# Kernel optimization log

Hardware: AMD Instinct MI355X
Metric: run time of the kernel (lower is better)

The kernel has to match this reference:

```python
import jax, jax.numpy as jnp
import numpy as np

DIM = 2048
LAT = 512          # dim / compression_factor
NH = 16
NKV = 4
HD = LAT // NH     # 32
KVD = NKV * HD     # 128
K = 3              # conv kernel
GAIN = 0.25
EPS = 1e-6
THETA = 10000.0


def _rms(x, g):
    x32 = x.astype(jnp.float32)
    r = jax.lax.rsqrt(jnp.mean(x32 * x32, axis=-1, keepdims=True) + EPS)
    return (x32 * r).astype(x.dtype) * g.astype(x.dtype)


def _causal_conv(x, w, groups):
    # x: [B,S,C], w: [C, C//groups, K]; left-pad K-1 == pad both + trim right
    xc = jnp.transpose(x, (0, 2, 1))
    y = jax.lax.conv_general_dilated(
        xc, w, window_strides=(1,), padding=[(K - 1, 0)],
        feature_group_count=groups, dimension_numbers=('NCH', 'OIH', 'NCH'))
    return jnp.transpose(y, (0, 2, 1))


def _rope_tables(S):
    freqs = 1.0 / THETA ** (jnp.arange(0, HD, 2, dtype=jnp.float32) / HD)
    t = jnp.arange(S, dtype=jnp.float32)
    f = jnp.outer(t, freqs)               # [S, HD/2]
    return jnp.cos(f), jnp.sin(f)


def _rope(x, cos, sin):
    # x: [B,H,S,HD]; interleaved even/odd rotation
    x1, x2 = x[..., ::2], x[..., 1::2]
    r1 = x1 * cos - x2 * sin
    r2 = x1 * sin + x2 * cos
    return jnp.stack([r1, r2], axis=-1).reshape(x.shape)


def setup_inputs() -> dict:
    key = jax.random.key(0)
    ks = jax.random.split(key, 8)
    s = 0.02
    return {
        'x': jax.random.normal(ks[0], (4, 2048, DIM), jnp.float32),
        'w_q': jax.random.normal(ks[1], (LAT, DIM), jnp.float32) * s,
        'w_k': jax.random.normal(ks[2], (KVD, DIM), jnp.float32) * s,
        'w_v': jax.random.normal(ks[3], (KVD, DIM), jnp.float32) * s,
        'g_latent': jnp.ones((LAT,), jnp.float32),
        'g_kv': jnp.ones((KVD,), jnp.float32),
        'conv_q_w': jax.random.normal(ks[4], (LAT, LAT // NH, K), jnp.float32) * s,
        'conv_k_w': jax.random.normal(ks[5], (KVD, KVD // NKV, K), jnp.float32) * s,
        'g_conv': jnp.ones((LAT,), jnp.float32),
        'g_kconv': jnp.ones((KVD,), jnp.float32),
        'g_postq': jnp.ones((LAT,), jnp.float32),
        'g_postk': jnp.ones((KVD,), jnp.float32),
        'key_temp': jnp.ones((1,), jnp.float32),
        'g_preout': jnp.ones((LAT,), jnp.float32),
        'w_o': jax.random.normal(ks[6], (DIM, LAT), jnp.float32) * s,
    }


def reference(x, w_q, w_k, w_v, g_latent, g_kv, conv_q_w, conv_k_w,
              g_conv, g_kconv, g_postq, g_postk, key_temp, g_preout, w_o):
    B, S, D = x.shape
    n_groups = NH // NKV

    q = _rms(x @ w_q.T, g_latent)          # [B,S,LAT]
    k = _rms(x @ w_k.T, g_kv)              # [B,S,KVD]
    v = _rms(x @ w_v.T, g_kv)
    q_pre, k_pre = q, k

    q = _rms(_causal_conv(q, conv_q_w, NH), g_conv)
    k = _rms(_causal_conv(k, conv_k_w, NKV), g_kconv)

    # qk-mean modulation (n_groups > 1 branch)
    q_mean = q_pre.reshape(B, S, NH, HD).mean(axis=2)    # [B,S,HD]
    k_mean = k_pre.reshape(B, S, NKV, HD).mean(axis=2)   # [B,S,HD]
    q = q + GAIN * jnp.broadcast_to(k_mean[:, :, None, :], (B, S, NH, HD)).reshape(B, S, LAT)
    k = k + GAIN * jnp.broadcast_to(q_mean[:, :, None, :], (B, S, NKV, HD)).reshape(B, S, KVD)

    q = _rms(q, g_postq)
    k = _rms(k, g_postk)

    q = q.reshape(B, S, NH, HD).transpose(0, 2, 1, 3)    # [B,NH,S,HD]
    k = k.reshape(B, S, NKV, HD).transpose(0, 2, 1, 3)   # [B,NKV,S,HD]
    v = v.reshape(B, S, NKV, HD).transpose(0, 2, 1, 3)

    # QK L2 norm with learnable key temperature
    sqrt_hd = jnp.sqrt(jnp.float32(HD))
    qn = jnp.maximum(jnp.linalg.norm(q, axis=-1, keepdims=True), 1e-12)
    kn = jnp.maximum(jnp.linalg.norm(k, axis=-1, keepdims=True), 1e-12)
    q = q / qn * sqrt_hd
    k = k / kn * sqrt_hd * key_temp[0]

    cos, sin = _rope_tables(S)
    q = _rope(q, cos, sin)
    k = _rope(k, cos, sin)

    # GQA expand kv heads
    k = jnp.broadcast_to(k[:, :, None], (B, NKV, n_groups, S, HD)).reshape(B, NH, S, HD)
    v = jnp.broadcast_to(v[:, :, None], (B, NKV, n_groups, S, HD)).reshape(B, NH, S, HD)

    scale = HD ** -0.5
    scores = jnp.einsum('bhqd,bhkd->bhqk', q, k) * scale
    causal = jnp.tril(jnp.ones((S, S), bool))
    scores = jnp.where(causal, scores, jnp.finfo(scores.dtype).min)
    attn = jax.nn.softmax(scores, axis=-1)
    out = jnp.einsum('bhqk,bhkd->bhqd', attn, v)

    out = out.transpose(0, 2, 1, 3).reshape(B, S, LAT)
    out = _rms(out, g_preout)
    return out @ w_o.T
```

## Files before the change

### kernel.cpp

```cpp
#include <hip/hip_runtime.h>
#include <hip/hip_bf16.h>
#include <math.h>

constexpr int S_LEN = 2048;
constexpr int B_SZ  = 4;
constexpr int NROWS = B_SZ * S_LEN;
constexpr float GAIN_  = 0.25f;
constexpr float EPS_   = 1e-6f;
constexpr float THETA_ = 10000.0f;
constexpr float LOG2E_ = 1.44269504f;

typedef __attribute__((ext_vector_type(8))) short short8;
typedef __attribute__((ext_vector_type(4))) short sshort4;
typedef __attribute__((ext_vector_type(4))) float float4v;

__device__ __forceinline__ short f2bs(float f) {
    __hip_bfloat16 h = __float2bfloat16(f);
    short r;
    __builtin_memcpy(&r, &h, 2);
    return r;
}

__device__ __forceinline__ float bs2f(short s) {
    unsigned u = ((unsigned)(unsigned short)s) << 16;
    float f;
    __builtin_memcpy(&f, &u, 4);
    return f;
}

__device__ __forceinline__ void async_copy16(const short* g, short* l) {
    __builtin_amdgcn_global_load_lds(
        (const __attribute__((address_space(1))) void*)g,
        (__attribute__((address_space(3))) void*)l, 16, 0, 0);
}

__device__ __forceinline__ int xcd_remap(int nwg) {
    int orig = blockIdx.x + gridDim.x * (blockIdx.y + gridDim.y * blockIdx.z);
    return (orig & 7) * (nwg >> 3) + (orig >> 3);
}

__device__ __forceinline__ float block_reduce_sum_256(float v, float* scratch) {
    __syncthreads();
    for (int off = 32; off > 0; off >>= 1)
        v += __shfl_down(v, off, 64);
    int lane = threadIdx.x & 63;
    int wid  = threadIdx.x >> 6;
    if (lane == 0) scratch[wid] = v;
    __syncthreads();
    return scratch[0] + scratch[1] + scratch[2] + scratch[3];
}

__device__ __forceinline__ void block_reduce_sum2_256(float& a, float& b, float* scratch) {
    __syncthreads();
    for (int off = 32; off > 0; off >>= 1) {
        a += __shfl_down(a, off, 64);
        b += __shfl_down(b, off, 64);
    }
    int lane = threadIdx.x & 63;
    int wid  = threadIdx.x >> 6;
    if (lane == 0) { scratch[wid] = a; scratch[4 + wid] = b; }
    __syncthreads();
    a = scratch[0] + scratch[1] + scratch[2] + scratch[3];
    b = scratch[4] + scratch[5] + scratch[6] + scratch[7];
}

__device__ __forceinline__ void block_reduce_sum3_256(float& a, float& b, float& c, float* scratch) {
    __syncthreads();
    for (int off = 32; off > 0; off >>= 1) {
        a += __shfl_down(a, off, 64);
        b += __shfl_down(b, off, 64);
        c += __shfl_down(c, off, 64);
    }
    int lane = threadIdx.x & 63;
    int wid  = threadIdx.x >> 6;
    if (lane == 0) { scratch[wid] = a; scratch[4 + wid] = b; scratch[8 + wid] = c; }
    __syncthreads();
    a = scratch[0] + scratch[1] + scratch[2] + scratch[3];
    b = scratch[4] + scratch[5] + scratch[6] + scratch[7];
    c = scratch[8] + scratch[9] + scratch[10] + scratch[11];
}

__global__ __launch_bounds__(256) void cvt_bf16(
    const float* __restrict__ src, short* __restrict__ dst, int n) {
    int i = (blockIdx.x * 256 + threadIdx.x) * 4;
    if (i >= n) return;
    float4 v = *(const float4*)(src + i);
    sshort4 o;
    o.x = f2bs(v.x); o.y = f2bs(v.y); o.z = f2bs(v.z); o.w = f2bs(v.w);
    *(sshort4*)(dst + i) = o;
}

__global__ __launch_bounds__(256) void cvt_weights(
    const float* __restrict__ wq, const float* __restrict__ wk,
    const float* __restrict__ wv, const float* __restrict__ wo,
    short* __restrict__ wqkvb, short* __restrict__ wob) {
    int i = (blockIdx.x * 256 + threadIdx.x) * 4;
    const float* src;
    short* dst;
    int j;
    if (i < 1048576)      { src = wq; dst = wqkvb + i; j = i; }
    else if (i < 1310720) { src = wk; dst = wqkvb + i; j = i - 1048576; }
    else if (i < 1572864) { src = wv; dst = wqkvb + i; j = i - 1310720; }
    else                  { src = wo; dst = wob + (i - 1572864); j = i - 1572864; }
    float4 v = *(const float4*)(src + j);
    sshort4 o;
    o.x = f2bs(v.x); o.y = f2bs(v.y); o.z = f2bs(v.z); o.w = f2bs(v.w);
    *(sshort4*)dst = o;
}

__global__ __launch_bounds__(256) void rope_tab(float* __restrict__ tab) {
    int i = blockIdx.x * 256 + threadIdx.x;
    int s = i >> 4, fi = i & 15;
    float freq = powf(THETA_, -(float)fi / 16.f);
    float sn, cs;
    sincosf((float)s * freq, &sn, &cs);
    tab[i * 2]     = cs;
    tab[i * 2 + 1] = sn;
}

__global__ __launch_bounds__(256) void gemm_bf16_mfma(
    const short* __restrict__ A, const short* __restrict__ B,
    float* __restrict__ C, int N, int K) {
    __shared__ short As[128 * 32];
    __shared__ short Bs[128 * 32];
    int tid = threadIdx.x;
    int wave = tid >> 6, lane = tid & 63;
    int wg = xcd_remap(gridDim.x * gridDim.y);
    int bx = wg % gridDim.x, by = wg / gridDim.x;
    int m0 = by * 128, n0 = bx * 128;
    int wm = (wave >> 1) * 64, wn = (wave & 1) * 64;
    int mrow = lane & 15, quad = lane >> 4;
    float4v acc[4][4] = {};
    for (int k0 = 0; k0 < K; k0 += 32) {
        __syncthreads();
#pragma unroll
        for (int p = 0; p < 2; ++p) {
            int f = p * 256 + tid;
            int row = f >> 2, ch = (f & 3) * 8;
            const short* ga = A + (size_t)(m0 + row) * K + k0 + ch;
            const short* gb = B + (size_t)(n0 + row) * K + k0 + ch;
            async_copy16(ga, As + p * 2048 + wave * 512);
            async_copy16(gb, Bs + p * 2048 + wave * 512);
        }
        __syncthreads();
        short8 af[4], bf[4];
#pragma unroll
        for (int i = 0; i < 4; ++i)
            af[i] = *(const short8*)&As[(wm + i * 16 + mrow) * 32 + quad * 8];
#pragma unroll
        for (int j = 0; j < 4; ++j)
            bf[j] = *(const short8*)&Bs[(wn + j * 16 + mrow) * 32 + quad * 8];
#pragma unroll
        for (int i = 0; i < 4; ++i)
#pragma unroll
            for (int j = 0; j < 4; ++j)
                acc[i][j] = __builtin_amdgcn_mfma_f32_16x16x32_bf16(af[i], bf[j], acc[i][j], 0, 0, 0);
    }
#pragma unroll
    for (int i = 0; i < 4; ++i)
#pragma unroll
        for (int r = 0; r < 4; ++r) {
            int m = m0 + wm + i * 16 + quad * 4 + r;
            float* crow = C + (size_t)m * N + n0 + wn;
#pragma unroll
            for (int j = 0; j < 4; ++j)
                crow[j * 16 + mrow] = acc[i][j][r];
        }
}

__global__ __launch_bounds__(256) void gemm_bf16_mfma_sk2(
    const short* __restrict__ A, const short* __restrict__ B,
    float* __restrict__ C0, float* __restrict__ C1, int N, int K) {
    __shared__ short As[128 * 32];
    __shared__ short Bs[128 * 32];
    int tid = threadIdx.x;
    int wave = tid >> 6, lane = tid & 63;
    int wg = xcd_remap(gridDim.x * gridDim.y * gridDim.z);
    int bx = wg % gridDim.x;
    int t  = wg / gridDim.x;
    int by = t % gridDim.y;
    int bz = t / gridDim.y;
    int m0 = by * 128, n0 = bx * 128;
    int wm = (wave >> 1) * 64, wn = (wave & 1) * 64;
    int mrow = lane & 15, quad = lane >> 4;
    int kh = K >> 1;
    int kbeg = bz * kh, kend = kbeg + kh;
    float* __restrict__ C = bz ? C1 : C0;
    float4v acc[4][4] = {};
    for (int k0 = kbeg; k0 < kend; k0 += 32) {
        __syncthreads();
#pragma unroll
        for (int p = 0; p < 2; ++p) {
            int f = p * 256 + tid;
            int row = f >> 2, ch = (f & 3) * 8;
            const short* ga = A + (size_t)(m0 + row) * K + k0 + ch;
            const short* gb = B + (size_t)(n0 + row) * K + k0 + ch;
            async_copy16(ga, As + p * 2048 + wave * 512);
            async_copy16(gb, Bs + p * 2048 + wave * 512);
        }
        __syncthreads();
        short8 af[4], bf[4];
#pragma unroll
        for (int i = 0; i < 4; ++i)
            af[i] = *(const short8*)&As[(wm + i * 16 + mrow) * 32 + quad * 8];
#pragma unroll
        for (int j = 0; j < 4; ++j)
            bf[j] = *(const short8*)&Bs[(wn + j * 16 + mrow) * 32 + quad * 8];
#pragma unroll
        for (int i = 0; i < 4; ++i)
#pragma unroll
            for (int j = 0; j < 4; ++j)
                acc[i][j] = __builtin_amdgcn_mfma_f32_16x16x32_bf16(af[i], bf[j], acc[i][j], 0, 0, 0);
    }
#pragma unroll
    for (int i = 0; i < 4; ++i)
#pragma unroll
        for (int r = 0; r < 4; ++r) {
            int m = m0 + wm + i * 16 + quad * 4 + r;
            float* crow = C + (size_t)m * N + n0 + wn;
#pragma unroll
            for (int j = 0; j < 4; ++j)
                crow[j * 16 + mrow] = acc[i][j][r];
        }
}

__global__ __launch_bounds__(256) void rms_qkv_means(
    float* __restrict__ qkv, const float* __restrict__ qkv2,
    const float* __restrict__ g_latent, const float* __restrict__ g_kv,
    float* __restrict__ qmean, float* __restrict__ kmean,
    short* __restrict__ vtb) {
    int row = blockIdx.x;
    int b = row >> 11, s = row & (S_LEN - 1);
    float* p = qkv + (size_t)row * 768;
    const float* p2 = qkv2 + (size_t)row * 768;
    __shared__ float sh[640];
    __shared__ float scratch[12];
    int tid = threadIdx.x;
    float v0 = p[tid] + p2[tid];
    float v1 = p[tid + 256] + p2[tid + 256];
    float v2 = p[tid + 512] + p2[tid + 512];
    float sq = v0 * v0 + v1 * v1;
    float sk = (tid < 128) ? v2 * v2 : 0.f;
    float sv = (tid >= 128) ? v2 * v2 : 0.f;
    block_reduce_sum3_256(sq, sk, sv, scratch);
    float rq = rsqrtf(sq / 512.f + EPS_);
    float q0 = v0 * rq * g_latent[tid];
    float q1 = v1 * rq * g_latent[tid + 256];
    p[tid] = q0; p[tid + 256] = q1;
    sh[tid] = q0; sh[tid + 256] = q1;
    if (tid < 128) {
        float rk = rsqrtf(sk / 128.f + EPS_);
        float kv = v2 * rk * g_kv[tid];
        p[512 + tid] = kv; sh[512 + tid] = kv;
    } else {
        float rv = rsqrtf(sv / 128.f + EPS_);
        float vv = v2 * rv * g_kv[tid - 128];
        int d_full = tid - 128;
        vtb[((size_t)(b * 4 + (d_full >> 5)) * 32 + (d_full & 31)) * S_LEN + s] = f2bs(vv);
    }
    __syncthreads();
    if (tid < 32) {
        float sm = 0.f;
#pragma unroll
        for (int h = 0; h < 16; ++h) sm += sh[h * 32 + tid];
        qmean[(size_t)row * 32 + tid] = sm * (1.f / 16.f);
    } else if (tid < 64) {
        int d = tid - 32;
        float sm = 0.f;
#pragma unroll
        for (int h = 0; h < 4; ++h) sm += sh[512 + h * 32 + d];
        kmean[(size_t)row * 32 + d] = sm * 0.25f;
    }
}

__global__ __launch_bounds__(256) void causal_conv32(
    const float* __restrict__ in, int ldin, int inoff,
    const float* __restrict__ w, float* __restrict__ out, int C) {
    int b = blockIdx.z, g = blockIdx.y, s0 = blockIdx.x * 32;
    __shared__ float wsh[32][3][32];
    __shared__ float ish[34][33];
    int tid = threadIdx.x;
    for (int i = tid; i < 32 * 96; i += 256) {
        int oc = i / 96, r = i % 96;
        wsh[r / 3][r % 3][oc] = w[(size_t)(g * 32 + oc) * 96 + r];
    }
    for (int i = tid; i < 34 * 32; i += 256) {
        int pp = i >> 5, ic = i & 31;
        int s = s0 - 2 + pp;
        ish[pp][ic] = (s >= 0) ? in[((size_t)b * S_LEN + s) * ldin + inoff + g * 32 + ic] : 0.f;
    }
    __syncthreads();
    int sl = tid >> 3, oc0 = (tid & 7) * 4;
    float acc[4] = {0.f, 0.f, 0.f, 0.f};
    for (int ic = 0; ic < 32; ++ic) {
        float x0 = ish[sl][ic], x1 = ish[sl + 1][ic], x2 = ish[sl + 2][ic];
#pragma unroll
        for (int j = 0; j < 4; ++j)
            acc[j] += x0 * wsh[ic][0][oc0 + j] + x1 * wsh[ic][1][oc0 + j] + x2 * wsh[ic][2][oc0 + j];
    }
    float* orow = out + ((size_t)b * S_LEN + s0 + sl) * C + g * 32 + oc0;
    orow[0] = acc[0]; orow[1] = acc[1]; orow[2] = acc[2]; orow[3] = acc[3];
}

__global__ __launch_bounds__(256) void mix_rows(
    const float* __restrict__ convq, const float* __restrict__ convk,
    const float* __restrict__ qmean, const float* __restrict__ kmean,
    const float* __restrict__ g_conv, const float* __restrict__ g_kconv,
    const float* __restrict__ g_postq, const float* __restrict__ g_postk,
    const float* __restrict__ key_temp, const float* __restrict__ rtab,
    short* __restrict__ qb, short* __restrict__ kb) {
    int row = blockIdx.x;
    int s = row & (S_LEN - 1);
    int tid = threadIdx.x;
    __shared__ float sh[640];
    __shared__ float scratch[8];
    __shared__ float hscale[20];
    float q0 = convq[(size_t)row * 512 + tid];
    float q1 = convq[(size_t)row * 512 + tid + 256];
    float k0 = (tid < 128) ? convk[(size_t)row * 128 + tid] : 0.f;
    float ssq = q0 * q0 + q1 * q1;
    float ssk = k0 * k0;
    block_reduce_sum2_256(ssq, ssk, scratch);
    float r1  = rsqrtf(ssq / 512.f + EPS_);
    float rk1 = rsqrtf(ssk / 128.f + EPS_);
    float km = kmean[(size_t)row * 32 + (tid & 31)];
    float a0 = q0 * r1 * g_conv[tid] + GAIN_ * km;
    float a1 = q1 * r1 * g_conv[tid + 256] + GAIN_ * km;
    float ak = 0.f;
    if (tid < 128) ak = k0 * rk1 * g_kconv[tid] + GAIN_ * qmean[(size_t)row * 32 + (tid & 31)];
    float ssq2 = a0 * a0 + a1 * a1;
    float ssk2 = ak * ak;
    block_reduce_sum2_256(ssq2, ssk2, scratch);
    float r2  = rsqrtf(ssq2 / 512.f + EPS_);
    float rk2 = rsqrtf(ssk2 / 128.f + EPS_);
    sh[tid] = a0 * r2 * g_postq[tid];
    sh[tid + 256] = a1 * r2 * g_postq[tid + 256];
    if (tid < 128) sh[512 + tid] = ak * rk2 * g_postk[tid];
    __syncthreads();
    if (tid < 16) {
        float ssh = 0.f;
        for (int d = 0; d < 32; ++d) { float x = sh[tid * 32 + d]; ssh += x * x; }
        hscale[tid] = LOG2E_ / fmaxf(sqrtf(ssh), 1e-12f);
    } else if (tid < 20) {
        int h = tid - 16;
        float ssh = 0.f;
        for (int d = 0; d < 32; ++d) { float x = sh[512 + h * 32 + d]; ssh += x * x; }
        hscale[tid] = sqrtf(32.f) / fmaxf(sqrtf(ssh), 1e-12f) * key_temp[0];
    }
    __syncthreads();
    {
        int i0 = tid * 2;
        int h = i0 >> 5;
        int fi = (i0 & 31) >> 1;
        float sc = hscale[h];
        float x1 = sh[i0] * sc, x2 = sh[i0 + 1] * sc;
        float2 cssn = *(const float2*)&rtab[((size_t)s * 16 + fi) * 2];
        float cs = cssn.x, sn = cssn.y;
        unsigned lo = (unsigned short)f2bs(x1 * cs - x2 * sn);
        unsigned hi = (unsigned short)f2bs(x1 * sn + x2 * cs);
        *(unsigned*)(qb + (size_t)row * 512 + i0) = lo | (hi << 16);
    }
    if (tid < 64) {
        int i0 = tid * 2;
        int h = i0 >> 5;
        int fi = (i0 & 31) >> 1;
        float sc = hscale[16 + h];
        float x1 = sh[512 + i0] * sc, x2 = sh[512 + i0 + 1] * sc;
        float2 cssn = *(const float2*)&rtab[((size_t)s * 16 + fi) * 2];
        float cs = cssn.x, sn = cssn.y;
        unsigned lo = (unsigned short)f2bs(x1 * cs - x2 * sn);
        unsigned hi = (unsigned short)f2bs(x1 * sn + x2 * cs);
        *(unsigned*)(kb + (size_t)row * 128 + i0) = lo | (hi << 16);
    }
}

__global__ __launch_bounds__(256) void attn_mfma(
    const short* __restrict__ qb, const short* __restrict__ kb,
    const short* __restrict__ vtb, short* __restrict__ obf,
    const float* __restrict__ key_temp) {
    int pair = blockIdx.x, h = blockIdx.y, b = blockIdx.z;
    int kvh = h >> 2;
    __shared__ short KF[2][2048];
    __shared__ short VF[2][2048];
    __shared__ __align__(16) short PF[4 * 16 * 72];
    int tid = threadIdx.x, wave = tid >> 6, lane = tid & 63;
    int cc = lane & 15, quad = lane >> 4;
    short* PFw = PF + wave * 16 * 72;
    int ldsoff = wave * 512;
    float shift2 = -5.6568543f * key_temp[0] * LOG2E_;
    float4v zinit = {shift2, shift2, shift2, shift2};
    short8 ones;
#pragma unroll
    for (int j = 0; j < 8; ++j) ones[j] = (short)0x3F80;

    const short* ksrc0 = kb +
        ((size_t)(b * S_LEN + wave * 16 + (tid & 15)) * 128
         + kvh * 32 + ((tid >> 4) & 3) * 8);
    const short* vsrc0 = vtb +
        ((size_t)((b * 4 + kvh) * 32 + (wave & 1) * 16 + (tid & 15)) * S_LEN
         + (tid >> 7) * 32 + ((tid >> 4) & 3) * 8);

    for (int half = 0; half < 2; ++half) {
        int qt = half ? (31 - pair) : pair;
        int s0 = qt * 64;
        short8 qfrag = *(const short8*)(qb +
            ((size_t)(b * S_LEN + s0 + wave * 16 + cc) * 512 + h * 32 + quad * 8));
        float4v accO[2];
        accO[0] = (float4v){0.f, 0.f, 0.f, 0.f};
        accO[1] = (float4v){0.f, 0.f, 0.f, 0.f};
        float4v accL = (float4v){0.f, 0.f, 0.f, 0.f};
        int qpos = s0 + wave * 16 + cc;
        const short* ksrc = ksrc0;
        const short* vsrc = vsrc0;
        int nkt = qt + 1;

        __syncthreads();
        int cur = 0;
        async_copy16(ksrc, KF[0] + ldsoff);
        async_copy16(vsrc, VF[0] + ldsoff);
        ksrc += 64 * 128;
        vsrc += 64;
        for (int kt = 0; kt < nkt; ++kt) {
            __syncthreads();
            if (kt + 1 < nkt) {
                async_copy16(ksrc, KF[cur ^ 1] + ldsoff);
                async_copy16(vsrc, VF[cur ^ 1] + ldsoff);
                ksrc += 64 * 128;
                vsrc += 64;
            }
            const short* KFc = KF[cur];
            const short* VFc = VF[cur];

            float4v st[4];
#pragma unroll
            for (int chunk = 0; chunk < 4; ++chunk) {
                short8 kfrag = *(const short8*)&KFc[chunk * 512 + lane * 8];
                st[chunk] = __builtin_amdgcn_mfma_f32_16x16x32_bf16(kfrag, qfrag, zinit, 0, 0, 0);
            }

            bool diag = (kt == qt);
#pragma unroll
            for (int chunk = 0; chunk < 4; ++chunk) {
                float pv[4];
#pragma unroll
                for (int r = 0; r < 4; ++r) {
                    float e = exp2f(st[chunk][r]);
                    if (diag) {
                        int kpos = kt * 64 + chunk * 16 + quad * 4 + r;
                        e = (kpos <= qpos) ? e : 0.f;
                    }
                    pv[r] = e;
                }
                unsigned u0, u1;
                asm("v_cvt_pk_bf16_f32 %0, %1, %2" : "=v"(u0) : "v"(pv[0]), "v"(pv[1]));
                asm("v_cvt_pk_bf16_f32 %0, %1, %2" : "=v"(u1) : "v"(pv[2]), "v"(pv[3]));
                *(uint2*)&PFw[cc * 72 + chunk * 16 + quad * 4] = make_uint2(u0, u1);
            }

#pragma unroll
            for (int kc = 0; kc < 2; ++kc) {
                short8 pfrag = *(const short8*)&PFw[cc * 72 + kc * 32 + quad * 8];
                accL = __builtin_amdgcn_mfma_f32_16x16x32_bf16(pfrag, ones, accL, 0, 0, 0);
#pragma unroll
                for (int dc = 0; dc < 2; ++dc) {
                    short8 vfrag = *(const short8*)&VFc[(kc * 2 + dc) * 512 + lane * 8];
                    accO[dc] = __builtin_amdgcn_mfma_f32_16x16x32_bf16(pfrag, vfrag, accO[dc], 0, 0, 0);
                }
            }
            cur ^= 1;
        }

#pragma unroll
        for (int r = 0; r < 4; ++r) {
            float linv = 1.f / accL[r];
            short* dst = obf +
                ((size_t)(b * S_LEN + s0 + wave * 16 + quad * 4 + r) * 512 + h * 32 + cc);
            dst[0]  = f2bs(accO[0][r] * linv);
            dst[16] = f2bs(accO[1][r] * linv);
        }
    }
}

__global__ __launch_bounds__(256) void rms_preout_bf16(
    const short* __restrict__ obf, const float* __restrict__ g,
    short* __restrict__ outb) {
    int row = blockIdx.x;
    __shared__ float scratch[4];
    int tid = threadIdx.x;
    unsigned pk = *(const unsigned*)(obf + (size_t)row * 512 + tid * 2);
    float v0 = bs2f((short)(pk & 0xFFFF));
    float v1 = bs2f((short)(pk >> 16));
    float ssq = block_reduce_sum_256(v0 * v0 + v1 * v1, scratch);
    float r = rsqrtf(ssq / 512.f + EPS_);
    unsigned lo = (unsigned short)f2bs(v0 * r * g[tid * 2]);
    unsigned hi = (unsigned short)f2bs(v1 * r * g[tid * 2 + 1]);
    *(unsigned*)(outb + (size_t)row * 512 + tid * 2) = lo | (hi << 16);
}

extern "C" void kernel_launch(void* const* d_in, const int* in_sizes, int n_in,
                              void* d_out, int out_size, void* d_ws, size_t ws_size,
                              hipStream_t stream) {
    (void)in_sizes; (void)n_in; (void)out_size; (void)ws_size;
    const float* x        = (const float*)d_in[0];
    const float* w_q      = (const float*)d_in[1];
    const float* w_k      = (const float*)d_in[2];
    const float* w_v      = (const float*)d_in[3];
    const float* g_latent = (const float*)d_in[4];
    const float* g_kv     = (const float*)d_in[5];
    const float* conv_q_w = (const float*)d_in[6];
    const float* conv_k_w = (const float*)d_in[7];
    const float* g_conv   = (const float*)d_in[8];
    const float* g_kconv  = (const float*)d_in[9];
    const float* g_postq  = (const float*)d_in[10];
    const float* g_postk  = (const float*)d_in[11];
    const float* key_temp = (const float*)d_in[12];
    const float* g_preout = (const float*)d_in[13];
    const float* w_o      = (const float*)d_in[14];
    float* out = (float*)d_out;

    char* ws = (char*)d_ws;
    const size_t R = NROWS;
    float* qkv   = (float*)ws;                        ws += R * 768 * 4;
    float* qmean = (float*)ws;                        ws += R * 32 * 4;
    float* kmean = (float*)ws;                        ws += R * 32 * 4;
    float* convq = (float*)ws;                        ws += R * 512 * 4;
    float* convk = (float*)ws;                        ws += R * 128 * 4;
    short* qbb   = (short*)ws;                        ws += R * 512 * 2;
    short* kbb   = (short*)ws;                        ws += R * 128 * 2;
    short* vtb   = (short*)ws;                        ws += R * 128 * 2;
    short* xb    = (short*)ws;                        ws += R * 2048 * 2;
    short* wqkvb = (short*)ws;                        ws += 768 * 2048 * 2;
    short* w_ob  = (short*)ws;                        ws += 2048 * 512 * 2;
    float* rtab  = (float*)ws;                        ws += 2048 * 16 * 2 * 4;
    float* qkv2  = convq;
    short* obf   = xb;
    short* attnb = xb + R * 512;

    dim3 blk(256);
    rope_tab<<<128, blk, 0, stream>>>(rtab);
    cvt_bf16<<<(NROWS * 2048) / 1024, blk, 0, stream>>>(x, xb, NROWS * 2048);
    cvt_weights<<<2560, blk, 0, stream>>>(w_q, w_k, w_v, w_o, wqkvb, w_ob);

    gemm_bf16_mfma_sk2<<<dim3(6, 64, 2), blk, 0, stream>>>(xb, wqkvb, qkv, qkv2, 768, 2048);
    rms_qkv_means<<<NROWS, blk, 0, stream>>>(qkv, qkv2, g_latent, g_kv, qmean, kmean, vtb);
    causal_conv32<<<dim3(64, 16, 4), blk, 0, stream>>>(qkv, 768, 0, conv_q_w, convq, 512);
    causal_conv32<<<dim3(64, 4, 4), blk, 0, stream>>>(qkv, 768, 512, conv_k_w, convk, 128);
    mix_rows<<<NROWS, blk, 0, stream>>>(convq, convk, qmean, kmean, g_conv, g_kconv,
                                        g_postq, g_postk, key_temp, rtab, qbb, kbb);
    attn_mfma<<<dim3(16, 16, 4), blk, 0, stream>>>(qbb, kbb, vtb, obf, key_temp);
    rms_preout_bf16<<<NROWS, blk, 0, stream>>>(obf, g_preout, attnb);
    gemm_bf16_mfma<<<dim3(16, 64), blk, 0, stream>>>(attnb, w_ob, out, 2048, 512);
}
```

Before: 365.7 us.

## Merge conversion and conv launches; triple-buffer K/V loads in attention

```diff
diff --git a/kernel.cpp b/kernel.cpp
--- a/kernel.cpp
+++ b/kernel.cpp
@@ -80,42 +80,42 @@
     c = scratch[8] + scratch[9] + scratch[10] + scratch[11];
 }
 
-__global__ __launch_bounds__(256) void cvt_bf16(
-    const float* __restrict__ src, short* __restrict__ dst, int n) {
-    int i = (blockIdx.x * 256 + threadIdx.x) * 4;
-    if (i >= n) return;
-    float4 v = *(const float4*)(src + i);
-    sshort4 o;
-    o.x = f2bs(v.x); o.y = f2bs(v.y); o.z = f2bs(v.z); o.w = f2bs(v.w);
-    *(sshort4*)(dst + i) = o;
-}
-
-__global__ __launch_bounds__(256) void cvt_weights(
+__global__ __launch_bounds__(256) void cvt_all(
+    const float* __restrict__ x, short* __restrict__ xb,
     const float* __restrict__ wq, const float* __restrict__ wk,
     const float* __restrict__ wv, const float* __restrict__ wo,
-    short* __restrict__ wqkvb, short* __restrict__ wob) {
-    int i = (blockIdx.x * 256 + threadIdx.x) * 4;
-    const float* src;
-    short* dst;
-    int j;
-    if (i < 1048576)      { src = wq; dst = wqkvb + i; j = i; }
-    else if (i < 1310720) { src = wk; dst = wqkvb + i; j = i - 1048576; }
-    else if (i < 1572864) { src = wv; dst = wqkvb + i; j = i - 1310720; }
-    else                  { src = wo; dst = wob + (i - 1572864); j = i - 1572864; }
-    float4 v = *(const float4*)(src + j);
-    sshort4 o;
-    o.x = f2bs(v.x); o.y = f2bs(v.y); o.z = f2bs(v.z); o.w = f2bs(v.w);
-    *(sshort4*)dst = o;
-}
-
-__global__ __launch_bounds__(256) void rope_tab(float* __restrict__ tab) {
-    int i = blockIdx.x * 256 + threadIdx.x;
-    int s = i >> 4, fi = i & 15;
-    float freq = powf(THETA_, -(float)fi / 16.f);
-    float sn, cs;
-    sincosf((float)s * freq, &sn, &cs);
-    tab[i * 2]     = cs;
-    tab[i * 2 + 1] = sn;
+    short* __restrict__ wqkvb, short* __restrict__ wob,
+    float* __restrict__ rtab) {
+    int blk = blockIdx.x;
+    int tid = threadIdx.x;
+    if (blk < 16384) {
+        int i = (blk * 256 + tid) * 4;
+        float4 v = *(const float4*)(x + i);
+        sshort4 o;
+        o.x = f2bs(v.x); o.y = f2bs(v.y); o.z = f2bs(v.z); o.w = f2bs(v.w);
+        *(sshort4*)(xb + i) = o;
+    } else if (blk < 16384 + 2560) {
+        int i = ((blk - 16384) * 256 + tid) * 4;
+        const float* src;
+        short* dst;
+        int j;
+        if (i < 1048576)      { src = wq; dst = wqkvb + i; j = i; }
+        else if (i < 1310720) { src = wk; dst = wqkvb + i; j = i - 1048576; }
+        else if (i < 1572864) { src = wv; dst = wqkvb + i; j = i - 1310720; }
+        else                  { src = wo; dst = wob + (i - 1572864); j = i - 1572864; }
+        float4 v = *(const float4*)(src + j);
+        sshort4 o;
+        o.x = f2bs(v.x); o.y = f2bs(v.y); o.z = f2bs(v.z); o.w = f2bs(v.w);
+        *(sshort4*)dst = o;
+    } else {
+        int i = (blk - 16384 - 2560) * 256 + tid;
+        int s = i >> 4, fi = i & 15;
+        float freq = powf(THETA_, -(float)fi / 16.f);
+        float sn, cs;
+        sincosf((float)s * freq, &sn, &cs);
+        rtab[i * 2]     = cs;
+        rtab[i * 2 + 1] = sn;
+    }
 }
 
 __global__ __launch_bounds__(256) void gemm_bf16_mfma(
@@ -273,10 +273,10 @@
     }
 }
 
-__global__ __launch_bounds__(256) void causal_conv32(
+__device__ __forceinline__ void conv32_body(
     const float* __restrict__ in, int ldin, int inoff,
-    const float* __restrict__ w, float* __restrict__ out, int C) {
-    int b = blockIdx.z, g = blockIdx.y, s0 = blockIdx.x * 32;
+    const float* __restrict__ w, float* __restrict__ out, int C, int g) {
+    int b = blockIdx.z, s0 = blockIdx.x * 32;
     __shared__ float wsh[32][3][32];
     __shared__ float ish[34][33];
     int tid = threadIdx.x;
@@ -300,6 +300,15 @@
     }
     float* orow = out + ((size_t)b * S_LEN + s0 + sl) * C + g * 32 + oc0;
     orow[0] = acc[0]; orow[1] = acc[1]; orow[2] = acc[2]; orow[3] = acc[3];
+}
+
+__global__ __launch_bounds__(256) void causal_conv_all(
+    const float* __restrict__ qkv, const float* __restrict__ conv_q_w,
+    const float* __restrict__ conv_k_w, float* __restrict__ convq,
+    float* __restrict__ convk) {
+    int y = blockIdx.y;
+    if (y < 16) conv32_body(qkv, 768, 0,   conv_q_w, convq, 512, y);
+    else        conv32_body(qkv, 768, 512, conv_k_w, convk, 128, y - 16);
 }
 
 __global__ __launch_bounds__(256) void mix_rows(
@@ -380,8 +389,8 @@
     const float* __restrict__ key_temp) {
     int pair = blockIdx.x, h = blockIdx.y, b = blockIdx.z;
     int kvh = h >> 2;
-    __shared__ short KF[2][2048];
-    __shared__ short VF[2][2048];
+    __shared__ short KF[3][2048];
+    __shared__ short VF[3][2048];
     __shared__ __align__(16) short PF[4 * 16 * 72];
     int tid = threadIdx.x, wave = tid >> 6, lane = tid & 63;
     int cc = lane & 15, quad = lane >> 4;
@@ -415,21 +424,29 @@
         int nkt = qt + 1;
 
         __syncthreads();
-        int cur = 0;
         async_copy16(ksrc, KF[0] + ldsoff);
         async_copy16(vsrc, VF[0] + ldsoff);
-        ksrc += 64 * 128;
-        vsrc += 64;
+        ksrc += 64 * 128; vsrc += 64;
+        if (nkt > 1) {
+            async_copy16(ksrc, KF[1] + ldsoff);
+            async_copy16(vsrc, VF[1] + ldsoff);
+            ksrc += 64 * 128; vsrc += 64;
+        }
+        int bi = 0;
         for (int kt = 0; kt < nkt; ++kt) {
-            __syncthreads();
-            if (kt + 1 < nkt) {
-                async_copy16(ksrc, KF[cur ^ 1] + ldsoff);
-                async_copy16(vsrc, VF[cur ^ 1] + ldsoff);
-                ksrc += 64 * 128;
-                vsrc += 64;
+            if (kt + 1 < nkt) asm volatile("s_waitcnt vmcnt(2)" ::: "memory");
+            else              asm volatile("s_waitcnt vmcnt(0)" ::: "memory");
+            __builtin_amdgcn_sched_barrier(0);
+            __builtin_amdgcn_s_barrier();
+            __builtin_amdgcn_sched_barrier(0);
+            if (kt + 2 < nkt) {
+                int bn = bi ? bi - 1 : 2;
+                async_copy16(ksrc, KF[bn] + ldsoff);
+                async_copy16(vsrc, VF[bn] + ldsoff);
+                ksrc += 64 * 128; vsrc += 64;
             }
-            const short* KFc = KF[cur];
-            const short* VFc = VF[cur];
+            const short* KFc = KF[bi];
+            const short* VFc = VF[bi];
 
             float4v st[4];
 #pragma unroll
@@ -467,7 +484,7 @@
                     accO[dc] = __builtin_amdgcn_mfma_f32_16x16x32_bf16(pfrag, vfrag, accO[dc], 0, 0, 0);
                 }
             }
-            cur ^= 1;
+            bi = (bi == 2) ? 0 : bi + 1;
         }
 
 #pragma unroll
@@ -537,14 +554,12 @@
     short* attnb = xb + R * 512;
 
     dim3 blk(256);
-    rope_tab<<<128, blk, 0, stream>>>(rtab);
-    cvt_bf16<<<(NROWS * 2048) / 1024, blk, 0, stream>>>(x, xb, NROWS * 2048);
-    cvt_weights<<<2560, blk, 0, stream>>>(w_q, w_k, w_v, w_o, wqkvb, w_ob);
-
+    cvt_all<<<16384 + 2560 + 128, blk, 0, stream>>>(x, xb, w_q, w_k, w_v, w_o,
+                                                    wqkvb, w_ob, rtab);
     gemm_bf16_mfma_sk2<<<dim3(6, 64, 2), blk, 0, stream>>>(xb, wqkvb, qkv, qkv2, 768, 2048);
     rms_qkv_means<<<NROWS, blk, 0, stream>>>(qkv, qkv2, g_latent, g_kv, qmean, kmean, vtb);
-    causal_conv32<<<dim3(64, 16, 4), blk, 0, stream>>>(qkv, 768, 0, conv_q_w, convq, 512);
-    causal_conv32<<<dim3(64, 4, 4), blk, 0, stream>>>(qkv, 768, 512, conv_k_w, convk, 128);
+    causal_conv_all<<<dim3(64, 20, 4), blk, 0, stream>>>(qkv, conv_q_w, conv_k_w,
+                                                         convq, convk);
     mix_rows<<<NROWS, blk, 0, stream>>>(convq, convk, qmean, kmean, g_conv, g_kconv,
                                         g_postq, g_postk, key_temp, rtab, qbb, kbb);
     attn_mfma<<<dim3(16, 16, 4), blk, 0, stream>>>(qbb, kbb, vtb, obf, key_temp);
```

Result: no change. 361.3 us (-1.2%).
